# Kernel tuning notes

Hardware: AMD Instinct MI355X
Metric: run time of the kernel (lower is better)

Reference implementation:

```python
import jax, jax.numpy as jnp
import numpy as np

NUM_HEADS = 16
HEAD_DIM = 64
G_CONST = 1.0        # phase='fluid'
CURVATURE = 0.15     # phase='fluid'
EPS = 1e-06


def setup_inputs() -> dict:
    key = jax.random.key(0)
    k1, k2, k3, k4, k5 = jax.random.split(key, 5)
    B, S, D = 4, 4096, 1024
    x = jax.random.normal(k1, (B, S, D), dtype=jnp.float32)
    W_qkv = jax.random.normal(k2, (D, 3 * D), dtype=jnp.float32) * 0.02
    b_qkv = jax.random.normal(k3, (3 * D,), dtype=jnp.float32) * 0.02
    W_out = jax.random.normal(k4, (D, D), dtype=jnp.float32) * 0.02
    b_out = jax.random.normal(k5, (D,), dtype=jnp.float32) * 0.02
    return {"x": x, "W_qkv": W_qkv, "b_qkv": b_qkv, "W_out": W_out, "b_out": b_out}


def reference(x, W_qkv, b_qkv, W_out, b_out):
    B, S, D = x.shape
    H, Hd = NUM_HEADS, HEAD_DIM
    # qkv projection -> (B, S, 3, H, Hd); heads are NOT transposed (faithful to source):
    # attention is computed among the H heads at each token position.
    qkv = (x @ W_qkv + b_qkv).reshape(B, S, 3, H, Hd)
    q, k, v = qkv[:, :, 0], qkv[:, :, 1], qkv[:, :, 2]  # each (B,S,H,Hd)

    # squared euclidean distances between head vectors (matmul-based cdist, clamped >= 0)
    q_sq = jnp.sum(q * q, axis=-1)                      # (B,S,H)
    k_sq = jnp.sum(k * k, axis=-1)                      # (B,S,H)
    qk = jnp.einsum('bshd,bsgd->bshg', q, k)            # (B,S,H,H)
    dist_sq = jnp.maximum(q_sq[..., :, None] + k_sq[..., None, :] - 2.0 * qk, 0.0)

    # curvature cosine modulation (curvature != 0 in 'fluid' phase)
    dist_sq = dist_sq * (1.0 + CURVATURE * jnp.cos(jnp.sqrt(dist_sq + EPS)))

    # gravitational forces: G * m_q m_k / (d^2 + eps)
    m_q = jnp.sqrt(q_sq)                                # (B,S,H)
    m_k = jnp.sqrt(k_sq)                                # (B,S,H)
    forces = G_CONST * (m_q[..., :, None] * m_k[..., None, :]) / (dist_sq + EPS)

    attn = jax.nn.softmax(forces, axis=-1)              # softmax over key-heads
    out = jnp.einsum('bshg,bsgd->bshd', attn, v).reshape(B, S, D)
    return out @ W_out + b_out
```

## Files before the change

### kernel.cpp

```cpp
#include <hip/hip_runtime.h>
#include <hip/hip_bf16.h>
#include <math.h>

#define M_TOTAL 16384
#define D_MODEL 1024
#define N_QKV   3072
#define CURV    0.15f
#define EPS_F   1e-6f

typedef __attribute__((ext_vector_type(8))) short short8v;
typedef __attribute__((ext_vector_type(4))) float f32x4;

__device__ __forceinline__ void gl_lds16(const void* g, void* l) {
    __builtin_amdgcn_global_load_lds(
        (const __attribute__((address_space(1))) void*)g,
        (__attribute__((address_space(3))) void*)l, 16, 0, 0);
}
__device__ __forceinline__ unsigned short f2bf_bits(float x) {
    __hip_bfloat16 t = __float2bfloat16(x);
    return *(unsigned short*)&t;
}
__device__ __forceinline__ float bf2f(unsigned short u) {
    return __uint_as_float(((unsigned)u) << 16);
}

__global__ __launch_bounds__(256)
void cast_f32_bf16(const float* __restrict__ in, unsigned short* __restrict__ out,
                   int ngroups)
{
    int i = blockIdx.x * 256 + threadIdx.x;
    if (i >= ngroups) return;
    float4 u = ((const float4*)in)[i];
    ushort4 r;
    r.x = f2bf_bits(u.x); r.y = f2bf_bits(u.y);
    r.z = f2bf_bits(u.z); r.w = f2bf_bits(u.w);
    ((ushort4*)out)[i] = r;
}

__global__ __launch_bounds__(256)
void transpose_cast(const float* __restrict__ W, unsigned short* __restrict__ Wt,
                    int K, int N)
{
    __shared__ float tile[32][33];
    const int n0 = blockIdx.x * 32;
    const int k0 = blockIdx.y * 32;
    const int tx = threadIdx.x & 31;
    const int ty = threadIdx.x >> 5;
    #pragma unroll
    for (int i = 0; i < 32; i += 8)
        tile[ty + i][tx] = W[(size_t)(k0 + ty + i) * N + n0 + tx];
    __syncthreads();
    #pragma unroll
    for (int i = 0; i < 32; i += 8)
        Wt[(size_t)(n0 + ty + i) * K + k0 + tx] = f2bf_bits(tile[tx][ty + i]);
}

template<int OUT_BF16>
__global__ __launch_bounds__(512, 2)
void gemm256_8ph(const unsigned short* __restrict__ A,
                 const unsigned short* __restrict__ Bt,
                 const float* __restrict__ bias,
                 void* __restrict__ Cout,
                 int M, int N, int K, int nbx)
{
    __shared__ __align__(16) short smem_s[65536];

    const int t    = threadIdx.x;
    const int w    = t >> 6;
    const int lane = t & 63;
    const int wm   = w >> 2;
    const int wn   = w & 3;
    const int lr   = lane & 15;
    const int hi   = lane >> 4;
    const int lo7  = lane & 7;

    const int nwg  = gridDim.x;
    const int orig = blockIdx.x;
    const int wgid = (orig & 7) * (nwg >> 3) + (orig >> 3);
    const int by = wgid / nbx, bx = wgid % nbx;
    const int bm0 = by * 256, bn0 = bx * 256;

    const int nt = K >> 6;

    const int srow = t >> 3;
    const int scol = ((t & 7) ^ (srow & 7)) * 8;
    const unsigned short* Ag = A  + (size_t)(bm0 + srow) * K + scol;
    const unsigned short* Bg = Bt + (size_t)(bn0 + srow) * K + scol;
    const int wbase = w * 1024;

    auto STAGE = [&](int which, int half, int tile) {
        const unsigned short* g0 = (which ? Bg : Ag)
                                 + (size_t)(half * 128) * K + (size_t)tile * 64;
        char* d0 = (char*)smem_s + ((tile & 1) * 65536 + which * 32768
                                    + half * 16384 + wbase);
        gl_lds16(g0,                d0);
        gl_lds16(g0 + (size_t)64*K, d0 + 8192);
    };

    short8v a[8][2], b[4][2];
    f32x4 acc[8][4] = {};

    auto LDA = [&](int buf, int m, int ks) {
        a[m][ks] = *(const short8v*)&smem_s[buf*32768 + wm*8192
                        + (m*16 + lr)*64 + (((ks*4 + hi) ^ lo7) * 8)];
    };
    auto LDB = [&](int buf, int n, int ks) {
        b[n][ks] = *(const short8v*)&smem_s[buf*32768 + 16384 + (wn>>1)*8192
                        + ((wn&1)*64 + n*16 + lr)*64 + (((ks*4 + hi) ^ lo7) * 8)];
    };
    auto QUAD = [&](int mlo, int nlo) {
        __builtin_amdgcn_s_setprio(1);
        #pragma unroll
        for (int mi = 0; mi < 4; ++mi)
            #pragma unroll
            for (int ni = 0; ni < 2; ++ni)
                #pragma unroll
                for (int ks = 0; ks < 2; ++ks)
                    acc[mlo+mi][nlo+ni] = __builtin_amdgcn_mfma_f32_16x16x32_bf16(
                        a[mlo+mi][ks], b[nlo+ni][ks], acc[mlo+mi][nlo+ni], 0, 0, 0);
        __builtin_amdgcn_s_setprio(0);
    };

    STAGE(0,0,0); STAGE(0,1,0); STAGE(1,0,0); STAGE(1,1,0);
    STAGE(0,0,1); STAGE(0,1,1); STAGE(1,0,1); STAGE(1,1,1);
    asm volatile("s_waitcnt vmcnt(8)" ::: "memory");
    __builtin_amdgcn_s_barrier();
    #pragma unroll
    for (int m = 0; m < 4; ++m) { LDA(0,m,0); LDA(0,m,1); }
    LDB(0,0,0); LDB(0,0,1); LDB(0,1,0); LDB(0,1,1);

    for (int T = 0; T < nt; ++T) {
        const int buf  = T & 1;
        const int nbuf = buf ^ 1;
        LDB(buf,2,0); LDB(buf,2,1); LDB(buf,3,0); LDB(buf,3,1);
        asm volatile("s_waitcnt lgkmcnt(4)" ::: "memory");
        __builtin_amdgcn_sched_barrier(0);
        QUAD(0,0);
        #pragma unroll
        for (int m = 4; m < 8; ++m) { LDA(buf,m,0); LDA(buf,m,1); }
        asm volatile("s_waitcnt lgkmcnt(8)" ::: "memory");
        __builtin_amdgcn_sched_barrier(0);
        QUAD(0,2);
        __builtin_amdgcn_s_barrier();
        if (T+2 < nt) { STAGE(1,0,T+2); STAGE(1,1,T+2); }
        asm volatile("s_waitcnt lgkmcnt(0)" ::: "memory");
        __builtin_amdgcn_sched_barrier(0);
        QUAD(4,0);
        __builtin_amdgcn_s_barrier();
        if (T+2 < nt) { STAGE(0,0,T+2); STAGE(0,1,T+2); }
        if (T+2 < nt) { asm volatile("s_waitcnt vmcnt(8)" ::: "memory"); }
        else          { asm volatile("s_waitcnt vmcnt(0)" ::: "memory"); }
        __builtin_amdgcn_s_barrier();
        if (T+1 < nt) {
            #pragma unroll
            for (int m = 0; m < 4; ++m) { LDA(nbuf,m,0); LDA(nbuf,m,1); }
            LDB(nbuf,0,0); LDB(nbuf,0,1); LDB(nbuf,1,0); LDB(nbuf,1,1);
        }
        __builtin_amdgcn_sched_barrier(0);
        QUAD(4,2);
    }

    const int r0 = bm0 + wm*128 + hi*4;
    const int cb = bn0 + wn*64 + lr;
    float bv[4];
    #pragma unroll
    for (int n = 0; n < 4; ++n) bv[n] = bias[cb + n*16];
    if (OUT_BF16) {
        unsigned short* Cb = (unsigned short*)Cout;
        #pragma unroll
        for (int m = 0; m < 8; ++m)
            #pragma unroll
            for (int j = 0; j < 4; ++j) {
                unsigned short* rp = Cb + (size_t)(r0 + m*16 + j) * N;
                #pragma unroll
                for (int n = 0; n < 4; ++n)
                    rp[cb + n*16] = f2bf_bits(acc[m][n][j] + bv[n]);
            }
    } else {
        float* Cf = (float*)Cout;
        #pragma unroll
        for (int m = 0; m < 8; ++m)
            #pragma unroll
            for (int j = 0; j < 4; ++j) {
                float* rp = Cf + (size_t)(r0 + m*16 + j) * N;
                #pragma unroll
                for (int n = 0; n < 4; ++n)
                    rp[cb + n*16] = acc[m][n][j] + bv[n];
            }
    }
}

__global__ __launch_bounds__(256)
void attn_heads_kernel(const unsigned short* __restrict__ qkv,
                       unsigned short* __restrict__ aout)
{
    __shared__ float qs[16][68], ks[16][68], vs[16][68];
    __shared__ float qsq[16], ksq[16];
    __shared__ float attn_s[16][17];

    const int p = blockIdx.x;
    const int t = threadIdx.x;
    const short8v* rowv = (const short8v*)(qkv + (size_t)p * N_QKV);

    for (int c = t; c < N_QKV / 8; c += 256) {
        short8v v = rowv[c];
        int e0  = c << 3;
        int sec = e0 >> 10;
        int h   = (e0 >> 6) & 15;
        int d   = e0 & 63;
        float* dst = (sec == 0) ? &qs[h][d] : (sec == 1) ? &ks[h][d] : &vs[h][d];
        #pragma unroll
        for (int i = 0; i < 8; ++i)
            dst[i] = bf2f((unsigned short)v[i]);
    }
    __syncthreads();

    if (t < 32) {
        int hh = t & 15;
        const float* src = (t < 16) ? qs[hh] : ks[hh];
        float s = 0.f;
        #pragma unroll
        for (int d0 = 0; d0 < 64; d0 += 4) {
            float4 u = *(const float4*)(src + d0);
            s = fmaf(u.x,u.x, fmaf(u.y,u.y, fmaf(u.z,u.z, fmaf(u.w,u.w, s))));
        }
        if (t < 16) qsq[hh] = s; else ksq[hh] = s;
    }

    const int h = t >> 4;
    const int g = t & 15;
    float dot = 0.f;
    {
        const float* qr = qs[h];
        const float* kr = ks[g];
        #pragma unroll
        for (int d0 = 0; d0 < 64; d0 += 4) {
            float4 a = *(const float4*)(qr + d0);
            float4 b = *(const float4*)(kr + d0);
            dot = fmaf(a.x,b.x, fmaf(a.y,b.y, fmaf(a.z,b.z, fmaf(a.w,b.w, dot))));
        }
    }
    __syncthreads();

    float dsq = fmaxf(qsq[h] + ksq[g] - 2.f * dot, 0.f);
    dsq = dsq * (1.f + CURV * cosf(sqrtf(dsq + EPS_F)));
    float force = sqrtf(qsq[h]) * sqrtf(ksq[g]) / (dsq + EPS_F);

    float m = force;
    #pragma unroll
    for (int off = 8; off >= 1; off >>= 1)
        m = fmaxf(m, __shfl_xor(m, off, 16));
    float e = expf(force - m);
    float ssum = e;
    #pragma unroll
    for (int off = 8; off >= 1; off >>= 1)
        ssum += __shfl_xor(ssum, off, 16);
    attn_s[h][g] = e / ssum;
    __syncthreads();

    const int d  = t & 63;
    const int hb = t >> 6;
    float o[4] = {0.f, 0.f, 0.f, 0.f};
    #pragma unroll
    for (int gg = 0; gg < 16; ++gg) {
        float vv = vs[gg][d];
        #pragma unroll
        for (int hh = 0; hh < 4; ++hh)
            o[hh] = fmaf(attn_s[hb + hh*4][gg], vv, o[hh]);
    }
    unsigned short* orow = aout + (size_t)p * D_MODEL;
    #pragma unroll
    for (int hh = 0; hh < 4; ++hh)
        orow[(hb + hh*4) * 64 + d] = f2bf_bits(o[hh]);
}

extern "C" void kernel_launch(void* const* d_in, const int* in_sizes, int n_in,
                              void* d_out, int out_size, void* d_ws, size_t ws_size,
                              hipStream_t stream)
{
    const float* x     = (const float*)d_in[0];
    const float* W_qkv = (const float*)d_in[1];
    const float* b_qkv = (const float*)d_in[2];
    const float* W_out = (const float*)d_in[3];
    const float* b_out = (const float*)d_in[4];
    float* out = (float*)d_out;

    char* ws = (char*)d_ws;
    unsigned short* qkvb = (unsigned short*)ws;
    unsigned short* xb   = (unsigned short*)(ws + (size_t)M_TOTAL * N_QKV * 2);
    unsigned short* ab   = xb;
    unsigned short* Wt1  = (unsigned short*)(ws + (size_t)M_TOTAL * N_QKV * 2
                                                + (size_t)M_TOTAL * D_MODEL * 2);
    unsigned short* Wt2  = Wt1 + (size_t)N_QKV * D_MODEL;

    {
        int ngroups = M_TOTAL * D_MODEL / 4;
        cast_f32_bf16<<<ngroups / 256, 256, 0, stream>>>(x, xb, ngroups);
    }
    {
        dim3 g(N_QKV / 32, D_MODEL / 32);
        transpose_cast<<<g, 256, 0, stream>>>(W_qkv, Wt1, D_MODEL, N_QKV);
        dim3 g2(D_MODEL / 32, D_MODEL / 32);
        transpose_cast<<<g2, 256, 0, stream>>>(W_out, Wt2, D_MODEL, D_MODEL);
    }

    {
        int nbx = N_QKV / 256;
        int nwg = (M_TOTAL / 256) * nbx;
        gemm256_8ph<1><<<nwg, 512, 0, stream>>>(xb, Wt1, b_qkv, qkvb,
                                                M_TOTAL, N_QKV, D_MODEL, nbx);
    }

    attn_heads_kernel<<<M_TOTAL, 256, 0, stream>>>(qkvb, ab);

    {
        int nbx = D_MODEL / 256;
        int nwg = (M_TOTAL / 256) * nbx;
        gemm256_8ph<0><<<nwg, 512, 0, stream>>>(ab, Wt2, b_out, out,
                                                M_TOTAL, D_MODEL, D_MODEL, nbx);
    }
}
```

Baseline: 221.4 us.

## Rewrite per-token head attention with wave-level MFMA and register shuffles

Replaces the per-token 256-thread block attention kernel, which staged q/k/v through shared memory with barriers, with a kernel that gives each token to one wavefront. QK^T and P·V are computed with bf16 16x16x32 MFMA instructions, and the softmax and norms are done in registers using cross-lane shuffles. The aim is to drop LDS traffic, the __syncthreads barriers, and the scalar FMA loops. In exchange, attention probabilities are rounded to bf16 before the P·V product, and the V operand is gathered with scalar 16-bit global loads.

```diff
diff --git a/kernel.cpp b/kernel.cpp
--- a/kernel.cpp
+++ b/kernel.cpp
@@ -191,87 +191,87 @@
 }
 
 __global__ __launch_bounds__(256)
-void attn_heads_kernel(const unsigned short* __restrict__ qkv,
-                       unsigned short* __restrict__ aout)
-{
-    __shared__ float qs[16][68], ks[16][68], vs[16][68];
-    __shared__ float qsq[16], ksq[16];
-    __shared__ float attn_s[16][17];
-
-    const int p = blockIdx.x;
-    const int t = threadIdx.x;
-    const short8v* rowv = (const short8v*)(qkv + (size_t)p * N_QKV);
-
-    for (int c = t; c < N_QKV / 8; c += 256) {
-        short8v v = rowv[c];
-        int e0  = c << 3;
-        int sec = e0 >> 10;
-        int h   = (e0 >> 6) & 15;
-        int d   = e0 & 63;
-        float* dst = (sec == 0) ? &qs[h][d] : (sec == 1) ? &ks[h][d] : &vs[h][d];
-        #pragma unroll
-        for (int i = 0; i < 8; ++i)
-            dst[i] = bf2f((unsigned short)v[i]);
-    }
-    __syncthreads();
-
-    if (t < 32) {
-        int hh = t & 15;
-        const float* src = (t < 16) ? qs[hh] : ks[hh];
-        float s = 0.f;
-        #pragma unroll
-        for (int d0 = 0; d0 < 64; d0 += 4) {
-            float4 u = *(const float4*)(src + d0);
-            s = fmaf(u.x,u.x, fmaf(u.y,u.y, fmaf(u.z,u.z, fmaf(u.w,u.w, s))));
+void attn_mfma_kernel(const unsigned short* __restrict__ qkv,
+                      unsigned short* __restrict__ aout)
+{
+    const int l  = threadIdx.x & 63;
+    const int wv = threadIdx.x >> 6;
+    const int p  = blockIdx.x * 4 + wv;
+    const int lr = l & 15;
+    const int hi = l >> 4;
+    const unsigned short* base = qkv + (size_t)p * N_QKV;
+
+    short8v qf0 = *(const short8v*)(base +        lr*64 +      hi*8);
+    short8v qf1 = *(const short8v*)(base +        lr*64 + 32 + hi*8);
+    short8v kf0 = *(const short8v*)(base + 1024 + lr*64 +      hi*8);
+    short8v kf1 = *(const short8v*)(base + 1024 + lr*64 + 32 + hi*8);
+
+    f32x4 s = {};
+    s = __builtin_amdgcn_mfma_f32_16x16x32_bf16(kf0, qf0, s, 0, 0, 0);
+    s = __builtin_amdgcn_mfma_f32_16x16x32_bf16(kf1, qf1, s, 0, 0, 0);
+
+    float qsq = 0.f, ksq = 0.f;
+    #pragma unroll
+    for (int i = 0; i < 8; ++i) {
+        float q0 = bf2f((unsigned short)qf0[i]), q1 = bf2f((unsigned short)qf1[i]);
+        float k0 = bf2f((unsigned short)kf0[i]), k1 = bf2f((unsigned short)kf1[i]);
+        qsq = fmaf(q0, q0, fmaf(q1, q1, qsq));
+        ksq = fmaf(k0, k0, fmaf(k1, k1, ksq));
+    }
+    qsq += __shfl_xor(qsq, 16); qsq += __shfl_xor(qsq, 32);
+    ksq += __shfl_xor(ksq, 16); ksq += __shfl_xor(ksq, 32);
+
+    const float mq = sqrtf(qsq);
+
+    float P[4];
+    #pragma unroll
+    for (int j = 0; j < 4; ++j) {
+        float ksg = __shfl(ksq, hi * 4 + j);
+        float dsq = fmaxf(qsq + ksg - 2.f * s[j], 0.f);
+        dsq = dsq * (1.f + CURV * cosf(sqrtf(dsq + EPS_F)));
+        P[j] = mq * sqrtf(ksg) / (dsq + EPS_F);
+    }
+    float mx = fmaxf(fmaxf(P[0], P[1]), fmaxf(P[2], P[3]));
+    mx = fmaxf(mx, __shfl_xor(mx, 16));
+    mx = fmaxf(mx, __shfl_xor(mx, 32));
+    float sm = 0.f;
+    #pragma unroll
+    for (int j = 0; j < 4; ++j) { P[j] = expf(P[j] - mx); sm += P[j]; }
+    sm += __shfl_xor(sm, 16); sm += __shfl_xor(sm, 32);
+    const float inv = 1.f / sm;
+
+    unsigned int w0 = (unsigned)f2bf_bits(P[0] * inv)
+                    | ((unsigned)f2bf_bits(P[1] * inv) << 16);
+    unsigned int w1 = (unsigned)f2bf_bits(P[2] * inv)
+                    | ((unsigned)f2bf_bits(P[3] * inv) << 16);
+    const int s0 = lr + (((2 * hi)     & 3) << 4);
+    const int s1 = lr + (((2 * hi + 1) & 3) << 4);
+    unsigned int a0 = __shfl((int)w0, s0), a1 = __shfl((int)w1, s0);
+    unsigned int a2 = __shfl((int)w0, s1), a3 = __shfl((int)w1, s1);
+    if (hi >= 2) { a0 = a1 = a2 = a3 = 0; }
+    unsigned int pa_u[4] = {a0, a1, a2, a3};
+    short8v pa = *(short8v*)pa_u;
+
+    const unsigned short* vb = base + 2048;
+    unsigned short* orow = aout + (size_t)p * D_MODEL;
+    #pragma unroll
+    for (int c = 0; c < 4; ++c) {
+        unsigned int bu[4];
+        #pragma unroll
+        for (int e2 = 0; e2 < 4; ++e2) {
+            int g0 = (hi * 8 + e2 * 2) & 15;
+            int g1 = (hi * 8 + e2 * 2 + 1) & 15;
+            unsigned int lo = vb[g0 * 64 + c * 16 + lr];
+            unsigned int hi16 = vb[g1 * 64 + c * 16 + lr];
+            bu[e2] = lo | (hi16 << 16);
         }
-        if (t < 16) qsq[hh] = s; else ksq[hh] = s;
-    }
-
-    const int h = t >> 4;
-    const int g = t & 15;
-    float dot = 0.f;
-    {
-        const float* qr = qs[h];
-        const float* kr = ks[g];
-        #pragma unroll
-        for (int d0 = 0; d0 < 64; d0 += 4) {
-            float4 a = *(const float4*)(qr + d0);
-            float4 b = *(const float4*)(kr + d0);
-            dot = fmaf(a.x,b.x, fmaf(a.y,b.y, fmaf(a.z,b.z, fmaf(a.w,b.w, dot))));
-        }
-    }
-    __syncthreads();
-
-    float dsq = fmaxf(qsq[h] + ksq[g] - 2.f * dot, 0.f);
-    dsq = dsq * (1.f + CURV * cosf(sqrtf(dsq + EPS_F)));
-    float force = sqrtf(qsq[h]) * sqrtf(ksq[g]) / (dsq + EPS_F);
-
-    float m = force;
-    #pragma unroll
-    for (int off = 8; off >= 1; off >>= 1)
-        m = fmaxf(m, __shfl_xor(m, off, 16));
-    float e = expf(force - m);
-    float ssum = e;
-    #pragma unroll
-    for (int off = 8; off >= 1; off >>= 1)
-        ssum += __shfl_xor(ssum, off, 16);
-    attn_s[h][g] = e / ssum;
-    __syncthreads();
-
-    const int d  = t & 63;
-    const int hb = t >> 6;
-    float o[4] = {0.f, 0.f, 0.f, 0.f};
-    #pragma unroll
-    for (int gg = 0; gg < 16; ++gg) {
-        float vv = vs[gg][d];
-        #pragma unroll
-        for (int hh = 0; hh < 4; ++hh)
-            o[hh] = fmaf(attn_s[hb + hh*4][gg], vv, o[hh]);
-    }
-    unsigned short* orow = aout + (size_t)p * D_MODEL;
-    #pragma unroll
-    for (int hh = 0; hh < 4; ++hh)
-        orow[(hb + hh*4) * 64 + d] = f2bf_bits(o[hh]);
+        short8v bv = *(short8v*)bu;
+        f32x4 o = {};
+        o = __builtin_amdgcn_mfma_f32_16x16x32_bf16(pa, bv, o, 0, 0, 0);
+        #pragma unroll
+        for (int j = 0; j < 4; ++j)
+            orow[(hi * 4 + j) * 64 + c * 16 + lr] = f2bf_bits(o[j]);
+    }
 }
 
 extern "C" void kernel_launch(void* const* d_in, const int* in_sizes, int n_in,
@@ -311,7 +311,7 @@
                                                 M_TOTAL, N_QKV, D_MODEL, nbx);
     }
 
-    attn_heads_kernel<<<M_TOTAL, 256, 0, stream>>>(qkvb, ab);
+    attn_mfma_kernel<<<M_TOTAL / 4, 256, 0, stream>>>(qkvb, ab);
 
     {
         int nbx = D_MODEL / 256;
```

After: 191.4 us. -13.6%, faster.
